# Optimization experiments

Measured on AMD Instinct MI355X. Metric: run time of the kernel, lower is better.

Reference implementation:

```python
import jax, jax.numpy as jnp
import numpy as np

N_NODES = 100000
N_EDGES = 1600000
N_GRAPHS = 128
ATOM_F = 92
BOND_F = 41
EMB = 64
HID = 128
CHG = 16
N_LAYERS = 3
EPS = 1e-5


def setup_inputs() -> dict:
    key = jax.random.key(0)
    ks = jax.random.split(key, 32)
    s = 0.05
    inp = {
        "x": jax.random.normal(ks[0], (N_NODES, ATOM_F), jnp.float32),
        "edge_attr": jax.random.uniform(ks[1], (N_EDGES, BOND_F), jnp.float32),
        "charge": jax.random.normal(ks[2], (N_GRAPHS,), jnp.float32),
        "edge_index": jax.random.randint(ks[3], (2, N_EDGES), 0, N_NODES),
        "batch": jnp.sort(jax.random.randint(ks[4], (N_NODES,), 0, N_GRAPHS)),
        # embeddings
        "W_charge": jax.random.normal(ks[5], (1, CHG), jnp.float32) * s,
        "b_charge": jnp.zeros((CHG,), jnp.float32),
        "W_atom": jax.random.normal(ks[6], (ATOM_F + CHG, EMB), jnp.float32) * s,
        "b_atom": jnp.zeros((EMB,), jnp.float32),
        "W_bond": jax.random.normal(ks[7], (BOND_F, EMB), jnp.float32) * s,
        "b_bond": jnp.zeros((EMB,), jnp.float32),
        # conv layers (stacked over layer dim)
        "conv_eW1": jax.random.normal(ks[8], (N_LAYERS, 3 * EMB, EMB), jnp.float32) * s,
        "conv_eb1": jnp.zeros((N_LAYERS, EMB), jnp.float32),
        "conv_eW2": jax.random.normal(ks[9], (N_LAYERS, EMB, EMB), jnp.float32) * s,
        "conv_eb2": jnp.zeros((N_LAYERS, EMB), jnp.float32),
        "conv_nW1": jax.random.normal(ks[10], (N_LAYERS, 2 * EMB, EMB), jnp.float32) * s,
        "conv_nb1": jnp.zeros((N_LAYERS, EMB), jnp.float32),
        "conv_nW2": jax.random.normal(ks[11], (N_LAYERS, EMB, EMB), jnp.float32) * s,
        "conv_nb2": jnp.zeros((N_LAYERS, EMB), jnp.float32),
        "bn_gamma": jnp.ones((N_LAYERS, EMB), jnp.float32),
        "bn_beta": jnp.zeros((N_LAYERS, EMB), jnp.float32),
        # predictor
        "pW1": jax.random.normal(ks[12], (EMB, HID), jnp.float32) * s,
        "pb1": jnp.zeros((HID,), jnp.float32),
        "pW2": jax.random.normal(ks[13], (HID, HID), jnp.float32) * s,
        "pb2": jnp.zeros((HID,), jnp.float32),
        "pW3": jax.random.normal(ks[14], (HID, 1), jnp.float32) * s,
        "pb3": jnp.zeros((1,), jnp.float32),
    }
    return inp


def reference(x, edge_attr, charge, W_charge, b_charge, W_atom, b_atom,
              W_bond, b_bond, conv_eW1, conv_eb1, conv_eW2, conv_eb2,
              conv_nW1, conv_nb1, conv_nW2, conv_nb2, bn_gamma, bn_beta,
              pW1, pb1, pW2, pb2, pW3, pb3, edge_index, batch):
    sp = jax.nn.softplus
    n_nodes = x.shape[0]
    n_graphs = charge.shape[0]

    # early charge integration: per-graph charge embedding broadcast to nodes
    charge_feat = charge[:, None] @ W_charge + b_charge          # [B, CHG]
    x = jnp.concatenate([x, charge_feat[batch]], axis=1)          # [N, ATOM_F+CHG]
    x = x @ W_atom + b_atom                                       # [N, EMB]
    ea = edge_attr @ W_bond + b_bond                              # [E, EMB]

    row, col = edge_index[0], edge_index[1]
    for i in range(conv_eW1.shape[0]):
        xr, xc = x[row], x[col]                                   # gathers [E, EMB]
        # edge update: MLP on [x_row, x_col, edge_attr]
        e_in = jnp.concatenate([xr, xc, ea], axis=1)              # [E, 3*EMB]
        ea = sp(e_in @ conv_eW1[i] + conv_eb1[i]) @ conv_eW2[i] + conv_eb2[i]
        # node messages: MLP on [x_row, new edge_attr]
        m_in = jnp.concatenate([xr, ea], axis=1)                  # [E, 2*EMB]
        msg = sp(m_in @ conv_nW1[i] + conv_nb1[i]) @ conv_nW2[i] + conv_nb2[i]
        x_new = jax.ops.segment_sum(msg, col, num_segments=n_nodes)
        # BatchNorm1d (training-mode batch stats, biased variance)
        mean = jnp.mean(x_new, axis=0)
        var = jnp.var(x_new, axis=0)
        x_new = (x_new - mean) * jax.lax.rsqrt(var + EPS) * bn_gamma[i] + bn_beta[i]
        x = sp(x_new) + x                                         # residual

    # global mean pool over graphs
    sums = jax.ops.segment_sum(x, batch, num_segments=n_graphs)   # [B, EMB]
    cnt = jax.ops.segment_sum(jnp.ones((n_nodes, 1), x.dtype), batch, num_segments=n_graphs)
    g = sums / jnp.maximum(cnt, 1.0)

    # predictor MLP (dropout is identity in eval mode)
    h = sp(g @ pW1 + pb1)
    h = sp(h @ pW2 + pb2)
    out = h @ pW3 + pb3                                           # [B, 1]
    return out.squeeze(-1)
```

## Files before the change

### kernel.cpp

```cpp
#include <hip/hip_runtime.h>
#include <math.h>

typedef short v8s __attribute__((ext_vector_type(8)));
typedef float v4f __attribute__((ext_vector_type(4)));
typedef unsigned int u32x4 __attribute__((ext_vector_type(4)));

__device__ __forceinline__ u32x4 nt_load4(const void* p) {
  return __builtin_nontemporal_load((const u32x4*)p);
}
__device__ __forceinline__ void nt_store4(void* p, u32x4 v) {
  __builtin_nontemporal_store(v, (u32x4*)p);
}

__device__ __forceinline__ float sp_f(float x) {
  return fmaxf(x, 0.0f) + 0.69314718056f * __log2f(1.0f + __expf(-fabsf(x)));
}

__device__ __forceinline__ unsigned short f2bf(float f) {
  union { float f; unsigned u; } x; x.f = f;
  unsigned r = (x.u + 0x7FFF + ((x.u >> 16) & 1)) >> 16;
  return (unsigned short)r;
}

__device__ __forceinline__ float bf2f(unsigned short h) {
  union { unsigned u; float f; } x; x.u = ((unsigned)h) << 16;
  return x.f;
}

__global__ __launch_bounds__(256) void k_prep_wfrag(
    const float* __restrict__ eW1, const float* __restrict__ eW2,
    const float* __restrict__ nW1, const float* __restrict__ nW2,
    const float* __restrict__ W_bond, unsigned short* __restrict__ wfrag) {
  if (blockIdx.x == 12) {
    unsigned short* out = wfrag + 12 * 4096;
    for (int f = threadIdx.x; f < 4096; f += 256) {
      int j = f & 7, ln = (f >> 3) & 63, kh = (f >> 9) & 1, ct = f >> 10;
      int k = kh * 32 + (ln >> 4) * 8 + j;
      int n = ct * 16 + (ln & 15);
      out[f] = (k < 41) ? f2bf(W_bond[k * 64 + n]) : 0;
    }
    return;
  }
  int i = blockIdx.x >> 2;
  int m = blockIdx.x & 3;
  const float* W;
  if (m == 0)      W = eW1 + (size_t)i * 192 * 64 + 128 * 64;
  else if (m == 1) W = eW2 + (size_t)i * 64 * 64;
  else if (m == 2) W = nW1 + (size_t)i * 128 * 64 + 64 * 64;
  else             W = nW2 + (size_t)i * 64 * 64;
  unsigned short* out = wfrag + ((size_t)i * 4 + m) * 4096;
  for (int f = threadIdx.x; f < 4096; f += 256) {
    int j = f & 7, ln = (f >> 3) & 63, kh = (f >> 9) & 1, ct = f >> 10;
    int k = kh * 32 + (ln >> 4) * 8 + j;
    int n = ct * 16 + (ln & 15);
    out[f] = f2bf(W[k * 64 + n]);
  }
}

__global__ __launch_bounds__(256) void k_embed_nodes(
    const float* __restrict__ x, const int* __restrict__ batch,
    const float* __restrict__ charge, const float* __restrict__ W_charge,
    const float* __restrict__ b_charge, const float* __restrict__ W_atom,
    const float* __restrict__ b_atom, float* __restrict__ xemb, int N) {
  __shared__ float sW[108 * 64];
  __shared__ float sX[128 * 92];
  __shared__ float sb[64];
  __shared__ float sWc[16];
  __shared__ float sbc[16];
  for (int i = threadIdx.x; i < 108 * 64; i += blockDim.x) sW[i] = W_atom[i];
  if (threadIdx.x < 64) sb[threadIdx.x] = b_atom[threadIdx.x];
  if (threadIdx.x < 16) {
    sWc[threadIdx.x] = W_charge[threadIdx.x];
    sbc[threadIdx.x] = b_charge[threadIdx.x];
  }
  int ntiles = (N + 127) >> 7;
  for (int tile = blockIdx.x; tile < ntiles; tile += gridDim.x) {
    int base = tile << 7;
    int cnt = N - base; if (cnt > 128) cnt = 128;
    __syncthreads();
    if (cnt == 128) {
      const u32x4* src = (const u32x4*)(x + (size_t)base * 92);
      for (int i = threadIdx.x; i < 2944; i += 256)
        ((u32x4*)sX)[i] = nt_load4(&src[i]);
    } else {
      for (int i = threadIdx.x; i < cnt * 92; i += 256)
        sX[i] = x[(size_t)base * 92 + i];
    }
    __syncthreads();
    int t = threadIdx.x;
    int node = t & 127, half = t >> 7;
    if (node < cnt) {
      int n = base + node;
      float acc[32];
#pragma unroll
      for (int j = 0; j < 32; ++j) acc[j] = sb[half * 32 + j];
      const float* xr = sX + node * 92;
      for (int k = 0; k < 92; ++k) {
        float a = xr[k];
        const float* wk = sW + k * 64 + half * 32;
#pragma unroll
        for (int j = 0; j < 32; ++j) acc[j] = fmaf(a, wk[j], acc[j]);
      }
      float ch = charge[batch[n]];
#pragma unroll
      for (int c = 0; c < 16; ++c) {
        float cf = fmaf(ch, sWc[c], sbc[c]);
        const float* wk = sW + (92 + c) * 64 + half * 32;
#pragma unroll
        for (int j = 0; j < 32; ++j) acc[j] = fmaf(cf, wk[j], acc[j]);
      }
      float* o = xemb + (size_t)n * 64 + half * 32;
#pragma unroll
      for (int q8 = 0; q8 < 8; ++q8)
        ((float4*)o)[q8] = make_float4(acc[4*q8], acc[4*q8+1], acc[4*q8+2], acc[4*q8+3]);
    }
  }
}

__global__ __launch_bounds__(256) void k_hist(const int* __restrict__ col,
                                              int* __restrict__ counts, int E) {
  int stride = gridDim.x * blockDim.x;
  for (int e = blockIdx.x * blockDim.x + threadIdx.x; e < E; e += stride)
    atomicAdd(&counts[col[e]], 1);
}

__global__ __launch_bounds__(256) void k_scan1(const int* __restrict__ counts,
                                               int* __restrict__ cursor,
                                               int* __restrict__ bsum, int N) {
  __shared__ int sd[2][256];
  int t = threadIdx.x;
  int i = blockIdx.x * 256 + t;
  int v = (i < N) ? counts[i] : 0;
  sd[0][t] = v;
  __syncthreads();
  int s = 0;
#pragma unroll
  for (int off = 1; off < 256; off <<= 1) {
    int nv = sd[s][t];
    if (t >= off) nv += sd[s][t - off];
    sd[s ^ 1][t] = nv;
    s ^= 1;
    __syncthreads();
  }
  if (i < N) cursor[i] = sd[s][t] - v;
  if (t == 255) bsum[blockIdx.x] = sd[s][255];
}

__global__ __launch_bounds__(256) void k_scan2(int* __restrict__ b, int NB) {
  __shared__ int sd[2][256];
  __shared__ int carry_s;
  int t = threadIdx.x;
  if (t == 0) carry_s = 0;
  __syncthreads();
  for (int base = 0; base < NB; base += 256) {
    int i = base + t;
    int v = (i < NB) ? b[i] : 0;
    sd[0][t] = v;
    __syncthreads();
    int s = 0;
#pragma unroll
    for (int off = 1; off < 256; off <<= 1) {
      int nv = sd[s][t];
      if (t >= off) nv += sd[s][t - off];
      sd[s ^ 1][t] = nv;
      s ^= 1;
      __syncthreads();
    }
    int c = carry_s;
    int tot = sd[s][255];
    if (i < NB) b[i] = sd[s][t] + c;
    __syncthreads();
    if (t == 0) carry_s = c + tot;
    __syncthreads();
  }
}

__global__ __launch_bounds__(256) void k_scatter(
    const int* __restrict__ row, const int* __restrict__ col,
    int* __restrict__ cursor, const int* __restrict__ bsum,
    int* __restrict__ pos, int* __restrict__ row_s, int* __restrict__ col_s,
    int E) {
  int stride = gridDim.x * blockDim.x;
  for (int e = blockIdx.x * blockDim.x + threadIdx.x; e < E; e += stride) {
    int c = col[e];
    int p = atomicAdd(&cursor[c], 1);
    p += (c >= 256) ? bsum[(c >> 8) - 1] : 0;
    pos[e] = p;
    row_s[p] = row[e];
    col_s[p] = c;
  }
}

__global__ __launch_bounds__(256) void k_embed_bonds_mfma(
    const float* __restrict__ eattr, const int* __restrict__ pos,
    const unsigned short* __restrict__ gWb, const float* __restrict__ b_bond,
    unsigned short* __restrict__ ea16, int E) {
  __shared__ unsigned short sA[128 * 64];
  __shared__ unsigned short sOut[128 * 64];
  __shared__ float sb[64];
  __shared__ int spos[128];
  int tid = threadIdx.x;
  int w = tid >> 6, l = tid & 63, q = l >> 4, c16 = l & 15;
  int rbase = w * 32;
  if (tid < 64) sb[tid] = b_bond[tid];
  {
    uint4 z = make_uint4(0, 0, 0, 0);
    for (int i = tid; i < 1024; i += 256) ((uint4*)sA)[i] = z;
  }
  int ntiles = (E + 127) >> 7;
  for (int tile = blockIdx.x; tile < ntiles; tile += gridDim.x) {
    int te = tile << 7;
    int cnt = E - te; if (cnt > 128) cnt = 128;
    __syncthreads();
    int nflt = cnt * 41;
    for (int i = tid; i < nflt; i += 256) {
      int r = i / 41, k = i - r * 41;
      float v = __builtin_nontemporal_load(&eattr[(size_t)te * 41 + i]);
      sA[r * 64 + (k ^ ((r & 7) << 3))] = f2bf(v);
    }
    if (tid < 128) spos[tid] = (te + tid < E) ? pos[te + tid] : -1;
    __syncthreads();
    v8s bfr[4][2], af[2][2];
    v4f acc[2][4];
    const v8s* wp_ = (const v8s*)gWb;
#pragma unroll
    for (int ct = 0; ct < 4; ++ct)
#pragma unroll
      for (int kh = 0; kh < 2; ++kh)
        bfr[ct][kh] = wp_[(ct * 2 + kh) * 64 + l];
#pragma unroll
    for (int rb = 0; rb < 2; ++rb)
#pragma unroll
      for (int kh = 0; kh < 2; ++kh) {
        int row_ = rbase + rb * 16 + c16;
        af[rb][kh] = *(const v8s*)&sA[row_ * 64 +
                                      ((kh * 32 + q * 8) ^ ((row_ & 7) << 3))];
      }
#pragma unroll
    for (int rb = 0; rb < 2; ++rb)
#pragma unroll
      for (int ct = 0; ct < 4; ++ct) {
        v4f a_ = {0.f, 0.f, 0.f, 0.f};
        a_ = __builtin_amdgcn_mfma_f32_16x16x32_bf16(af[rb][0], bfr[ct][0], a_, 0, 0, 0);
        a_ = __builtin_amdgcn_mfma_f32_16x16x32_bf16(af[rb][1], bfr[ct][1], a_, 0, 0, 0);
        acc[rb][ct] = a_;
      }
#pragma unroll
    for (int rb = 0; rb < 2; ++rb)
#pragma unroll
      for (int ct = 0; ct < 4; ++ct) {
        int n = ct * 16 + c16;
#pragma unroll
        for (int r = 0; r < 4; ++r) {
          float v = acc[rb][ct][r] + sb[n];
          int row = rbase + rb * 16 + q * 4 + r;
          sOut[row * 64 + (n ^ ((row & 7) << 3))] = f2bf(v);
        }
      }
    __syncthreads();
    for (int i = tid; i < 1024; i += 256) {
      int r = i >> 3, cc = i & 7;
      int p = spos[r];
      if (p >= 0) {
        u32x4 d = *(const u32x4*)&sOut[r * 64 + ((cc * 8) ^ ((r & 7) << 3))];
        nt_store4(&ea16[(size_t)p * 64 + cc * 8], d);
      }
    }
  }
}

__device__ __forceinline__ void node_pre_body(
    const float* __restrict__ xr, const float* sWa, const float* sWb,
    const float* sWp, unsigned short* __restrict__ up16,
    unsigned short* __restrict__ v16, int n) {
  const float4* xr4 = (const float4*)xr;
  float u[64], p[64];
#pragma unroll
  for (int j = 0; j < 64; ++j) { u[j] = 0.f; p[j] = 0.f; }
  for (int k4 = 0; k4 < 16; ++k4) {
    float4 av = xr4[k4];
    const float* wa = sWa + k4 * 256;
    const float* wp = sWp + k4 * 256;
#pragma unroll
    for (int j = 0; j < 64; ++j) u[j] = fmaf(av.x, wa[j], u[j]);
#pragma unroll
    for (int j = 0; j < 64; ++j) p[j] = fmaf(av.x, wp[j], p[j]);
#pragma unroll
    for (int j = 0; j < 64; ++j) u[j] = fmaf(av.y, wa[64 + j], u[j]);
#pragma unroll
    for (int j = 0; j < 64; ++j) p[j] = fmaf(av.y, wp[64 + j], p[j]);
#pragma unroll
    for (int j = 0; j < 64; ++j) u[j] = fmaf(av.z, wa[128 + j], u[j]);
#pragma unroll
    for (int j = 0; j < 64; ++j) p[j] = fmaf(av.z, wp[128 + j], p[j]);
#pragma unroll
    for (int j = 0; j < 64; ++j) u[j] = fmaf(av.w, wa[192 + j], u[j]);
#pragma unroll
    for (int j = 0; j < 64; ++j) p[j] = fmaf(av.w, wp[192 + j], p[j]);
  }
  unsigned short* o = up16 + (size_t)n * 128;
#pragma unroll
  for (int q8 = 0; q8 < 8; ++q8) {
    unsigned short tmp[8];
#pragma unroll
    for (int j = 0; j < 8; ++j) {
      int i = q8 * 8 + j;
      tmp[j] = f2bf(u[((i & 3) << 4) | (i >> 2)]);
    }
    *(uint4*)&o[q8 * 8] = *(uint4*)tmp;
  }
#pragma unroll
  for (int q8 = 0; q8 < 8; ++q8) {
    unsigned short tmp[8];
#pragma unroll
    for (int j = 0; j < 8; ++j) {
      int i = q8 * 8 + j;
      tmp[j] = f2bf(p[((i & 3) << 4) | (i >> 2)]);
    }
    *(uint4*)&o[64 + q8 * 8] = *(uint4*)tmp;
  }
  float vv[64];
#pragma unroll
  for (int j = 0; j < 64; ++j) vv[j] = 0.f;
  for (int k4 = 0; k4 < 16; ++k4) {
    float4 av = xr4[k4];
    const float* wb = sWb + k4 * 256;
#pragma unroll
    for (int j = 0; j < 64; ++j) vv[j] = fmaf(av.x, wb[j], vv[j]);
#pragma unroll
    for (int j = 0; j < 64; ++j) vv[j] = fmaf(av.y, wb[64 + j], vv[j]);
#pragma unroll
    for (int j = 0; j < 64; ++j) vv[j] = fmaf(av.z, wb[128 + j], vv[j]);
#pragma unroll
    for (int j = 0; j < 64; ++j) vv[j] = fmaf(av.w, wb[192 + j], vv[j]);
  }
  unsigned short* ov = v16 + (size_t)n * 64;
#pragma unroll
  for (int q8 = 0; q8 < 8; ++q8) {
    unsigned short tmp[8];
#pragma unroll
    for (int j = 0; j < 8; ++j) {
      int i = q8 * 8 + j;
      tmp[j] = f2bf(vv[((i & 3) << 4) | (i >> 2)]);
    }
    *(uint4*)&ov[q8 * 8] = *(uint4*)tmp;
  }
}

__global__ __launch_bounds__(256) void k_node_pre(
    const float* __restrict__ xemb, const float* __restrict__ eW1,
    const float* __restrict__ nW1, unsigned short* __restrict__ up16,
    unsigned short* __restrict__ v16, float* __restrict__ xnew, int N) {
  __shared__ float sWa[64 * 64];
  __shared__ float sWb[64 * 64];
  __shared__ float sWp[64 * 64];
  for (int i = threadIdx.x; i < 64 * 64; i += blockDim.x) {
    sWa[i] = eW1[i];
    sWb[i] = eW1[64 * 64 + i];
    sWp[i] = nW1[i];
  }
  __syncthreads();
  int stride = gridDim.x * blockDim.x;
  float4 z = make_float4(0.f, 0.f, 0.f, 0.f);
  for (int n = blockIdx.x * blockDim.x + threadIdx.x; n < N; n += stride) {
    node_pre_body(xemb + (size_t)n * 64, sWa, sWb, sWp, up16, v16, n);
    float4* xz = (float4*)(xnew + (size_t)n * 64);
#pragma unroll
    for (int q = 0; q < 16; ++q) xz[q] = z;
  }
}

__global__ __launch_bounds__(256) void k_bn_pre(
    float* __restrict__ xemb, float* __restrict__ xnew,
    const float* __restrict__ bnacc, const float* __restrict__ gamma,
    const float* __restrict__ beta, const float* __restrict__ eW1n,
    const float* __restrict__ nW1n, unsigned short* __restrict__ up16,
    unsigned short* __restrict__ v16, int N) {
  __shared__ float sWa[64 * 64];
  __shared__ float sWb[64 * 64];
  __shared__ float sWp[64 * 64];
  __shared__ float sscale[64], sshift[64];
  for (int i = threadIdx.x; i < 64 * 64; i += blockDim.x) {
    sWa[i] = eW1n[i];
    sWb[i] = eW1n[64 * 64 + i];
    sWp[i] = nW1n[i];
  }
  if (threadIdx.x < 64) {
    float inv = 1.0f / (float)N;
    float m = bnacc[threadIdx.x] * inv;
    float var = bnacc[64 + threadIdx.x] * inv - m * m;
    float rs = rsqrtf(var + 1e-5f);
    float g = gamma[threadIdx.x];
    sscale[threadIdx.x] = rs * g;
    sshift[threadIdx.x] = beta[threadIdx.x] - m * rs * g;
  }
  __syncthreads();
  int stride = gridDim.x * blockDim.x;
  float4 z = make_float4(0.f, 0.f, 0.f, 0.f);
  for (int n = blockIdx.x * blockDim.x + threadIdx.x; n < N; n += stride) {
    float* xr = xemb + (size_t)n * 64;
    float4* xnrow = (float4*)(xnew + (size_t)n * 64);
#pragma unroll
    for (int q = 0; q < 16; ++q) {
      float4 xn4 = xnrow[q];
      float4 xo4 = ((const float4*)xr)[q];
      xo4.x += sp_f(fmaf(xn4.x, sscale[4*q+0], sshift[4*q+0]));
      xo4.y += sp_f(fmaf(xn4.y, sscale[4*q+1], sshift[4*q+1]));
      xo4.z += sp_f(fmaf(xn4.z, sscale[4*q+2], sshift[4*q+2]));
      xo4.w += sp_f(fmaf(xn4.w, sscale[4*q+3], sshift[4*q+3]));
      ((float4*)xr)[q] = xo4;
      xnrow[q] = z;
    }
    node_pre_body(xr, sWa, sWb, sWp, up16, v16, n);
  }
}

#define READ_FRAGS(P)                                                        \
  {                                                                          \
    const v8s* wp_ = (const v8s*)gWf + (P) * 512;                            \
    _Pragma("unroll") for (int ct = 0; ct < 4; ++ct)                         \
        _Pragma("unroll") for (int kh = 0; kh < 2; ++kh)                     \
            bfr[ct][kh] = wp_[(ct * 2 + kh) * 64 + l];                       \
    {                                                                        \
      int row_ = rbase + c16;                                                \
      _Pragma("unroll") for (int kh = 0; kh < 2; ++kh)                       \
        af[kh] = *(const v8s*)&sA[row_ * 64 +                                \
                                  ((kh * 32 + q * 8) ^ ((row_ & 7) << 3))];  \
    }                                                                        \
  }

#define DO_MFMA()                                                            \
  _Pragma("unroll") for (int ct = 0; ct < 4; ++ct) {                         \
    v4f a_ = {0.f, 0.f, 0.f, 0.f};                                           \
    a_ = __builtin_amdgcn_mfma_f32_16x16x32_bf16(af[0], bfr[ct][0], a_,      \
                                                 0, 0, 0);                   \
    a_ = __builtin_amdgcn_mfma_f32_16x16x32_bf16(af[1], bfr[ct][1], a_,      \
                                                 0, 0, 0);                   \
    acc[ct] = a_;                                                            \
  }

__global__ __launch_bounds__(512, 4) void k_edge_mfma(
    const int* __restrict__ row_s, const int* __restrict__ col_s,
    unsigned short* __restrict__ ea16, const unsigned short* __restrict__ up16,
    const unsigned short* __restrict__ v16,
    const unsigned short* __restrict__ gWf, const float* __restrict__ eb1,
    const float* __restrict__ eb2, const float* __restrict__ nb1,
    const float* __restrict__ nb2, float* __restrict__ xnew,
    float* __restrict__ bnacc, int E, int store_ea) {
  __shared__ __align__(16) unsigned char smem[65536];
  unsigned short* sA = (unsigned short*)smem;
  float* msgb        = (float*)smem;
  float* sBb         = (float*)(smem + 32768);
  int* scol          = (int*)(smem + 33792);

  int tid = threadIdx.x;
  int te = blockIdx.x * 128;
  int w = tid >> 6, l = tid & 63, q = l >> 4, c16 = l & 15;
  int rbase = w * 16;

  if (blockIdx.x == 0 && tid < 128) bnacc[tid] = 0.0f;

  int rid[4], cid[4], eid[4];
#pragma unroll
  for (int r = 0; r < 4; ++r) {
    int e = te + rbase + q * 4 + r;
    eid[r] = e;
    int ec = e < E ? e : E - 1;
    rid[r] = row_s[ec];
    cid[r] = col_s[ec];
  }
  ushort4 uu_pf[4], vv_pf[4];
#pragma unroll
  for (int r = 0; r < 4; ++r) {
    uu_pf[r] = *(const ushort4*)&up16[(size_t)rid[r] * 128 + c16 * 4];
    vv_pf[r] = *(const ushort4*)&v16[(size_t)cid[r] * 64 + c16 * 4];
  }

  if (tid < 64) {
    sBb[0 * 64 + tid] = eb1[tid];
    sBb[1 * 64 + tid] = eb2[tid];
    sBb[2 * 64 + tid] = nb1[tid];
    sBb[3 * 64 + tid] = nb2[tid];
  }
  if (tid < 128) {
    int e = te + tid;
    scol[tid] = col_s[e < E ? e : E - 1];
  }
  for (int i = tid; i < 1024; i += 512) {
    int r = i >> 3, cc = i & 7;
    int e = te + r;
    if (e >= E) e = E - 1;
    u32x4 d = nt_load4(&ea16[(size_t)e * 64 + cc * 8]);
    *(u32x4*)&sA[r * 64 + ((cc * 8) ^ ((r & 7) << 3))] = d;
  }

  v8s af[2];
  v8s bfr[4][2];
  v4f acc[4];

  __syncthreads();

  READ_FRAGS(0);
  DO_MFMA();
  ushort4 pp_pf[4];
#pragma unroll
  for (int r = 0; r < 4; ++r)
    pp_pf[r] = *(const ushort4*)&up16[(size_t)rid[r] * 128 + 64 + c16 * 4];
#pragma unroll
  for (int r = 0; r < 4; ++r) {
    const unsigned short* up_ = (const unsigned short*)&uu_pf[r];
    const unsigned short* vp_ = (const unsigned short*)&vv_pf[r];
    int row = rbase + q * 4 + r;
#pragma unroll
    for (int ct = 0; ct < 4; ++ct) {
      int n = ct * 16 + c16;
      float t = acc[ct][r] + sBb[n] + bf2f(up_[ct]) + bf2f(vp_[ct]);
      t = sp_f(t);
      sA[row * 64 + (n ^ ((row & 7) << 3))] = f2bf(t);
    }
  }

  READ_FRAGS(1);
  DO_MFMA();
#pragma unroll
  for (int ct = 0; ct < 4; ++ct) {
    int n = ct * 16 + c16;
#pragma unroll
    for (int r = 0; r < 4; ++r) {
      float en = acc[ct][r] + sBb[64 + n];
      int row = rbase + q * 4 + r;
      sA[row * 64 + (n ^ ((row & 7) << 3))] = f2bf(en);
    }
  }
  if (store_ea) {
    __syncthreads();
    for (int i = tid; i < 1024; i += 512) {
      int r = i >> 3, cc = i & 7;
      if (te + r < E) {
        u32x4 d = *(const u32x4*)&sA[r * 64 + ((cc * 8) ^ ((r & 7) << 3))];
        nt_store4(&ea16[(size_t)(te + r) * 64 + cc * 8], d);
      }
    }
    __syncthreads();
  }

  READ_FRAGS(2);
  DO_MFMA();
#pragma unroll
  for (int r = 0; r < 4; ++r) {
    const unsigned short* pp_ = (const unsigned short*)&pp_pf[r];
    int row = rbase + q * 4 + r;
#pragma unroll
    for (int ct = 0; ct < 4; ++ct) {
      int n = ct * 16 + c16;
      float t2 = acc[ct][r] + sBb[128 + n] + bf2f(pp_[ct]);
      t2 = sp_f(t2);
      sA[row * 64 + (n ^ ((row & 7) << 3))] = f2bf(t2);
    }
  }

  READ_FRAGS(3);
  __syncthreads();
  DO_MFMA();
#pragma unroll
  for (int ct = 0; ct < 4; ++ct) {
    int n = ct * 16 + c16;
#pragma unroll
    for (int r = 0; r < 4; ++r) {
      float msg = acc[ct][r] + sBb[192 + n];
      int row = rbase + q * 4 + r;
      msgb[row * 64 + n] = (eid[r] < E) ? msg : 0.0f;
    }
  }
  __syncthreads();

  int nrows = E - te;
  if (nrows > 128) nrows = 128;
  for (int r0 = w; r0 < nrows; r0 += 8) {
    int c0 = scol[r0];
    if (r0 > 0 && scol[r0 - 1] == c0) continue;
    float s = 0.0f;
    int r = r0;
    do {
      s += msgb[r * 64 + l];
      ++r;
    } while (r < nrows && scol[r] == c0);
    if (r0 > 0 && r < nrows)
      xnew[(size_t)c0 * 64 + l] = s;
    else
      atomicAdd(&xnew[(size_t)c0 * 64 + l], s);
  }
}

__global__ __launch_bounds__(256) void k_bn_stats(
    const float* __restrict__ xnew, float* __restrict__ bnacc, int N) {
  int t = threadIdx.x;
  int ch = t & 63;
  int sl = t >> 6;
  float s = 0.f, s2 = 0.f;
  for (int n = blockIdx.x * 4 + sl; n < N; n += gridDim.x * 4) {
    float v = xnew[(size_t)n * 64 + ch];
    s += v;
    s2 = fmaf(v, v, s2);
  }
  __shared__ float red[256], red2[256];
  red[t] = s;
  red2[t] = s2;
  __syncthreads();
  if (sl == 0) {
    s = red[ch] + red[64 + ch] + red[128 + ch] + red[192 + ch];
    s2 = red2[ch] + red2[64 + ch] + red2[128 + ch] + red2[192 + ch];
    atomicAdd(&bnacc[ch], s);
    atomicAdd(&bnacc[64 + ch], s2);
  }
}

__device__ __forceinline__ int lbound(const int* a, int n, int key) {
  int lo = 0, hi = n;
  while (lo < hi) {
    int mid = (lo + hi) >> 1;
    if (a[mid] < key) lo = mid + 1; else hi = mid;
  }
  return lo;
}

__global__ __launch_bounds__(256) void k_pool_pred_bn(
    const float* __restrict__ x, const float* __restrict__ xnew,
    const float* __restrict__ bnacc, const float* __restrict__ gamma,
    const float* __restrict__ beta, const int* __restrict__ batch, int N,
    const float* __restrict__ pW1, const float* __restrict__ pb1,
    const float* __restrict__ pW2, const float* __restrict__ pb2,
    const float* __restrict__ pW3, const float* __restrict__ pb3,
    float* __restrict__ out) {
  __shared__ float sscale[64], sshift[64];
  int t = threadIdx.x;
  if (t < 64) {
    float inv = 1.0f / (float)N;
    float m = bnacc[t] * inv;
    float var = bnacc[64 + t] * inv - m * m;
    float rs = rsqrtf(var + 1e-5f);
    float g = gamma[t];
    sscale[t] = rs * g;
    sshift[t] = beta[t] - m * rs * g;
  }
  __syncthreads();
  int b = blockIdx.x;
  int lo = lbound(batch, N, b);
  int hi = lbound(batch, N, b + 1);
  int ch = t & 63;
  int sl = t >> 6;
  float sc = sscale[ch], sh = sshift[ch];
  float s = 0.f;
  for (int n = lo + sl; n < hi; n += 4) {
    float xv = x[(size_t)n * 64 + ch];
    float xn = xnew[(size_t)n * 64 + ch];
    s += xv + sp_f(fmaf(xn, sc, sh));
  }
  __shared__ float red4[4][64];
  __shared__ float sg[64];
  __shared__ float sh1[128];
  __shared__ float red[128];
  red4[sl][ch] = s;
  __syncthreads();
  if (t < 64) {
    float tot = red4[0][t] + red4[1][t] + red4[2][t] + red4[3][t];
    float cnt = (float)(hi - lo);
    sg[t] = tot / fmaxf(cnt, 1.0f);
  }
  __syncthreads();
  if (t < 128) {
    float h = pb1[t];
    for (int k = 0; k < 64; ++k) h = fmaf(sg[k], pW1[k * 128 + t], h);
    sh1[t] = sp_f(h);
  }
  __syncthreads();
  if (t < 128) {
    float h = pb2[t];
    for (int k = 0; k < 128; ++k) h = fmaf(sh1[k], pW2[k * 128 + t], h);
    red[t] = sp_f(h) * pW3[t];
  }
  __syncthreads();
  for (int off = 64; off > 0; off >>= 1) {
    if (t < off) red[t] += red[t + off];
    __syncthreads();
  }
  if (t == 0) out[b] = red[0] + pb3[0];
}

extern "C" void kernel_launch(void* const* d_in, const int* in_sizes, int n_in,
                              void* d_out, int out_size, void* d_ws, size_t ws_size,
                              hipStream_t stream) {
  const float* x         = (const float*)d_in[0];
  const float* edge_attr = (const float*)d_in[1];
  const float* charge    = (const float*)d_in[2];
  const int*   eidx      = (const int*)d_in[3];
  const int*   batch     = (const int*)d_in[4];
  const float* W_charge  = (const float*)d_in[5];
  const float* b_charge  = (const float*)d_in[6];
  const float* W_atom    = (const float*)d_in[7];
  const float* b_atom    = (const float*)d_in[8];
  const float* W_bond    = (const float*)d_in[9];
  const float* b_bond    = (const float*)d_in[10];
  const float* eW1 = (const float*)d_in[11];
  const float* eb1 = (const float*)d_in[12];
  const float* eW2 = (const float*)d_in[13];
  const float* eb2 = (const float*)d_in[14];
  const float* nW1 = (const float*)d_in[15];
  const float* nb1 = (const float*)d_in[16];
  const float* nW2 = (const float*)d_in[17];
  const float* nb2 = (const float*)d_in[18];
  const float* gam = (const float*)d_in[19];
  const float* bet = (const float*)d_in[20];
  const float* pW1 = (const float*)d_in[21];
  const float* pb1 = (const float*)d_in[22];
  const float* pW2 = (const float*)d_in[23];
  const float* pb2 = (const float*)d_in[24];
  const float* pW3 = (const float*)d_in[25];
  const float* pb3 = (const float*)d_in[26];

  int N = in_sizes[4];
  int E = in_sizes[3] / 2;
  int B = in_sizes[2];
  const int* row = eidx;
  const int* col = eidx + E;

  char* wptr = (char*)d_ws;
  unsigned short* ea16 = (unsigned short*)wptr; wptr += (((size_t)E * 64 * 2 + 255) & ~255ull);
  unsigned short* up16 = (unsigned short*)wptr; wptr += (((size_t)N * 128 * 2 + 255) & ~255ull);
  unsigned short* v16  = (unsigned short*)wptr; wptr += (((size_t)N * 64 * 2 + 255) & ~255ull);
  unsigned short* wfrag = (unsigned short*)wptr; wptr += 13 * 4096 * 2;
  float* xemb = (float*)wptr; wptr += (size_t)N * 64 * 4;
  float* xnew = (float*)wptr; wptr += (size_t)N * 64 * 4;
  float* bnacc = (float*)wptr; wptr += 256 * 4;
  int* counts = (int*)wptr;   wptr += (size_t)N * 4;
  int* cursor = (int*)wptr;   wptr += (size_t)N * 4;
  int* bsum = (int*)wptr;     wptr += 4096;
  int* pos = (int*)wptr;      wptr += (size_t)E * 4;
  int* row_s = (int*)wptr;    wptr += (size_t)E * 4;
  int* col_s = (int*)wptr;    wptr += (size_t)E * 4;

  int NB = (N + 255) / 256;

  k_prep_wfrag<<<13, 256, 0, stream>>>(eW1, eW2, nW1, nW2, W_bond, wfrag);
  hipMemsetAsync(counts, 0, (size_t)N * 4, stream);
  k_hist<<<2048, 256, 0, stream>>>(col, counts, E);
  k_scan1<<<NB, 256, 0, stream>>>(counts, cursor, bsum, N);
  k_scan2<<<1, 256, 0, stream>>>(bsum, NB);
  k_scatter<<<2048, 256, 0, stream>>>(row, col, cursor, bsum, pos, row_s,
                                      col_s, E);

  int ntilesN = (N + 127) / 128;
  k_embed_nodes<<<ntilesN, 256, 0, stream>>>(x, batch, charge, W_charge,
                                             b_charge, W_atom, b_atom, xemb, N);
  k_embed_bonds_mfma<<<2048, 256, 0, stream>>>(edge_attr, pos,
                                               wfrag + 12 * 4096, b_bond,
                                               ea16, E);
  k_node_pre<<<NB, 256, 0, stream>>>(xemb, eW1, nW1, up16, v16, xnew, N);

  int gridE = (E + 127) / 128;
  for (int i = 0; i < 3; ++i) {
    k_edge_mfma<<<gridE, 512, 0, stream>>>(
        row_s, col_s, ea16, up16, v16, wfrag + (size_t)i * 16384,
        eb1 + (size_t)i * 64, eb2 + (size_t)i * 64, nb1 + (size_t)i * 64,
        nb2 + (size_t)i * 64, xnew, bnacc, E, (i < 2) ? 1 : 0);
    k_bn_stats<<<1024, 256, 0, stream>>>(xnew, bnacc, N);
    if (i < 2) {
      k_bn_pre<<<NB, 256, 0, stream>>>(
          xemb, xnew, bnacc, gam + (size_t)i * 64, bet + (size_t)i * 64,
          eW1 + (size_t)(i + 1) * 192 * 64, nW1 + (size_t)(i + 1) * 128 * 64,
          up16, v16, N);
    }
  }

  k_pool_pred_bn<<<B, 256, 0, stream>>>(xemb, xnew, bnacc, gam + 2 * 64,
                                        bet + 2 * 64, batch, N, pW1, pb1,
                                        pW2, pb2, pW3, pb3, (float*)d_out);
}
```

Measured before the change: 2.040 ms.

## Process two edge tiles per block with double-buffered LDS and cross-tile prefetch

Each edge-kernel block now handles two consecutive 128-edge tiles instead of one, and the grid is halved to match. Both tiles' edge features are loaded into separate LDS buffers up front. The gathered node features for the second tile are prefetched while the first tile's MFMA chain runs. The aim is to hide gather and load latency and amortize per-block setup such as bias loads and bnacc init. The cost is more live registers for the prefetch arrays and half as many blocks to spread across CUs, which may reduce latency hiding from occupancy.

New measurement: 2.175 ms. 1.07x slower.

```diff
diff --git a/kernel.cpp b/kernel.cpp
--- a/kernel.cpp
+++ b/kernel.cpp
@@ -415,7 +415,7 @@
   }
 }
 
-#define READ_FRAGS(P)                                                        \
+#define RFRAGS(P, SAX)                                                       \
   {                                                                          \
     const v8s* wp_ = (const v8s*)gWf + (P) * 512;                            \
     _Pragma("unroll") for (int ct = 0; ct < 4; ++ct)                         \
@@ -424,7 +424,7 @@
     {                                                                        \
       int row_ = rbase + c16;                                                \
       _Pragma("unroll") for (int kh = 0; kh < 2; ++kh)                       \
-        af[kh] = *(const v8s*)&sA[row_ * 64 +                                \
+        af[kh] = *(const v8s*)&(SAX)[row_ * 64 +                             \
                                   ((kh * 32 + q * 8) ^ ((row_ & 7) << 3))];  \
     }                                                                        \
   }
@@ -448,32 +448,39 @@
     const float* __restrict__ nb2, float* __restrict__ xnew,
     float* __restrict__ bnacc, int E, int store_ea) {
   __shared__ __align__(16) unsigned char smem[65536];
-  unsigned short* sA = (unsigned short*)smem;
+  unsigned short* sA0 = (unsigned short*)smem;
   float* msgb        = (float*)smem;
   float* sBb         = (float*)(smem + 32768);
   int* scol          = (int*)(smem + 33792);
+  unsigned short* sA1 = (unsigned short*)(smem + 34816);
 
   int tid = threadIdx.x;
-  int te = blockIdx.x * 128;
   int w = tid >> 6, l = tid & 63, q = l >> 4, c16 = l & 15;
   int rbase = w * 16;
 
   if (blockIdx.x == 0 && tid < 128) bnacc[tid] = 0.0f;
 
-  int rid[4], cid[4], eid[4];
+  int te[2];
+  te[0] = blockIdx.x * 256;
+  te[1] = te[0] + 128;
+
+  int ridA[2][4], cidA[2][4], eidA[2][4];
+#pragma unroll
+  for (int tt = 0; tt < 2; ++tt)
+#pragma unroll
+    for (int r = 0; r < 4; ++r) {
+      int e = te[tt] + rbase + q * 4 + r;
+      eidA[tt][r] = e;
+      int ec = e < E ? e : E - 1;
+      ridA[tt][r] = row_s[ec];
+      cidA[tt][r] = col_s[ec];
+    }
+
+  ushort4 uuA[2][4], vvA[2][4], ppA[2][4];
 #pragma unroll
   for (int r = 0; r < 4; ++r) {
-    int e = te + rbase + q * 4 + r;
-    eid[r] = e;
-    int ec = e < E ? e : E - 1;
-    rid[r] = row_s[ec];
-    cid[r] = col_s[ec];
-  }
-  ushort4 uu_pf[4], vv_pf[4];
-#pragma unroll
-  for (int r = 0; r < 4; ++r) {
-    uu_pf[r] = *(const ushort4*)&up16[(size_t)rid[r] * 128 + c16 * 4];
-    vv_pf[r] = *(const ushort4*)&v16[(size_t)cid[r] * 64 + c16 * 4];
+    uuA[0][r] = *(const ushort4*)&up16[(size_t)ridA[0][r] * 128 + c16 * 4];
+    vvA[0][r] = *(const ushort4*)&v16[(size_t)cidA[0][r] * 64 + c16 * 4];
   }
 
   if (tid < 64) {
@@ -482,16 +489,19 @@
     sBb[2 * 64 + tid] = nb1[tid];
     sBb[3 * 64 + tid] = nb2[tid];
   }
-  if (tid < 128) {
-    int e = te + tid;
+  if (tid < 256) {
+    int tt = tid >> 7;
+    int e = te[tt] + (tid & 127);
     scol[tid] = col_s[e < E ? e : E - 1];
   }
-  for (int i = tid; i < 1024; i += 512) {
-    int r = i >> 3, cc = i & 7;
-    int e = te + r;
+  for (int i = tid; i < 2048; i += 512) {
+    int tt = i >> 10, ii = i & 1023;
+    int r = ii >> 3, cc = ii & 7;
+    int e = te[tt] + r;
     if (e >= E) e = E - 1;
     u32x4 d = nt_load4(&ea16[(size_t)e * 64 + cc * 8]);
-    *(u32x4*)&sA[r * 64 + ((cc * 8) ^ ((r & 7) << 3))] = d;
+    unsigned short* sAx = tt ? sA1 : sA0;
+    *(u32x4*)&sAx[r * 64 + ((cc * 8) ^ ((r & 7) << 3))] = d;
   }
 
   v8s af[2];
@@ -500,95 +510,109 @@
 
   __syncthreads();
 
-  READ_FRAGS(0);
-  DO_MFMA();
-  ushort4 pp_pf[4];
-#pragma unroll
-  for (int r = 0; r < 4; ++r)
-    pp_pf[r] = *(const ushort4*)&up16[(size_t)rid[r] * 128 + 64 + c16 * 4];
-#pragma unroll
-  for (int r = 0; r < 4; ++r) {
-    const unsigned short* up_ = (const unsigned short*)&uu_pf[r];
-    const unsigned short* vp_ = (const unsigned short*)&vv_pf[r];
-    int row = rbase + q * 4 + r;
+#pragma unroll
+  for (int tt = 0; tt < 2; ++tt) {
+    if (tt == 1 && te[1] >= E) break;
+    unsigned short* sAx = tt ? sA1 : sA0;
+    int* scl = scol + tt * 128;
+
+    RFRAGS(0, sAx);
+    DO_MFMA();
+#pragma unroll
+    for (int r = 0; r < 4; ++r)
+      ppA[tt][r] =
+          *(const ushort4*)&up16[(size_t)ridA[tt][r] * 128 + 64 + c16 * 4];
+    if (tt == 0) {
+#pragma unroll
+      for (int r = 0; r < 4; ++r) {
+        uuA[1][r] = *(const ushort4*)&up16[(size_t)ridA[1][r] * 128 + c16 * 4];
+        vvA[1][r] = *(const ushort4*)&v16[(size_t)cidA[1][r] * 64 + c16 * 4];
+      }
+    }
+#pragma unroll
+    for (int r = 0; r < 4; ++r) {
+      const unsigned short* up_ = (const unsigned short*)&uuA[tt][r];
+      const unsigned short* vp_ = (const unsigned short*)&vvA[tt][r];
+      int row = rbase + q * 4 + r;
+#pragma unroll
+      for (int ct = 0; ct < 4; ++ct) {
+        int n = ct * 16 + c16;
+        float t = acc[ct][r] + sBb[n] + bf2f(up_[ct]) + bf2f(vp_[ct]);
+        t = sp_f(t);
+        sAx[row * 64 + (n ^ ((row & 7) << 3))] = f2bf(t);
+      }
+    }
+
+    RFRAGS(1, sAx);
+    DO_MFMA();
 #pragma unroll
     for (int ct = 0; ct < 4; ++ct) {
       int n = ct * 16 + c16;
-      float t = acc[ct][r] + sBb[n] + bf2f(up_[ct]) + bf2f(vp_[ct]);
-      t = sp_f(t);
-      sA[row * 64 + (n ^ ((row & 7) << 3))] = f2bf(t);
-    }
-  }
-
-  READ_FRAGS(1);
-  DO_MFMA();
-#pragma unroll
-  for (int ct = 0; ct < 4; ++ct) {
-    int n = ct * 16 + c16;
+#pragma unroll
+      for (int r = 0; r < 4; ++r) {
+        float en = acc[ct][r] + sBb[64 + n];
+        int row = rbase + q * 4 + r;
+        sAx[row * 64 + (n ^ ((row & 7) << 3))] = f2bf(en);
+      }
+    }
+    if (store_ea) {
+      __syncthreads();
+      for (int i = tid; i < 1024; i += 512) {
+        int r = i >> 3, cc = i & 7;
+        if (te[tt] + r < E) {
+          u32x4 d = *(const u32x4*)&sAx[r * 64 + ((cc * 8) ^ ((r & 7) << 3))];
+          nt_store4(&ea16[(size_t)(te[tt] + r) * 64 + cc * 8], d);
+        }
+      }
+      __syncthreads();
+    }
+
+    RFRAGS(2, sAx);
+    DO_MFMA();
 #pragma unroll
     for (int r = 0; r < 4; ++r) {
-      float en = acc[ct][r] + sBb[64 + n];
+      const unsigned short* pp_ = (const unsigned short*)&ppA[tt][r];
       int row = rbase + q * 4 + r;
-      sA[row * 64 + (n ^ ((row & 7) << 3))] = f2bf(en);
-    }
-  }
-  if (store_ea) {
-    __syncthreads();
-    for (int i = tid; i < 1024; i += 512) {
-      int r = i >> 3, cc = i & 7;
-      if (te + r < E) {
-        u32x4 d = *(const u32x4*)&sA[r * 64 + ((cc * 8) ^ ((r & 7) << 3))];
-        nt_store4(&ea16[(size_t)(te + r) * 64 + cc * 8], d);
-      }
-    }
-    __syncthreads();
-  }
-
-  READ_FRAGS(2);
-  DO_MFMA();
-#pragma unroll
-  for (int r = 0; r < 4; ++r) {
-    const unsigned short* pp_ = (const unsigned short*)&pp_pf[r];
-    int row = rbase + q * 4 + r;
+#pragma unroll
+      for (int ct = 0; ct < 4; ++ct) {
+        int n = ct * 16 + c16;
+        float t2 = acc[ct][r] + sBb[128 + n] + bf2f(pp_[ct]);
+        t2 = sp_f(t2);
+        sAx[row * 64 + (n ^ ((row & 7) << 3))] = f2bf(t2);
+      }
+    }
+
+    RFRAGS(3, sAx);
+    __syncthreads();
+    DO_MFMA();
 #pragma unroll
     for (int ct = 0; ct < 4; ++ct) {
       int n = ct * 16 + c16;
-      float t2 = acc[ct][r] + sBb[128 + n] + bf2f(pp_[ct]);
-      t2 = sp_f(t2);
-      sA[row * 64 + (n ^ ((row & 7) << 3))] = f2bf(t2);
-    }
-  }
-
-  READ_FRAGS(3);
-  __syncthreads();
-  DO_MFMA();
-#pragma unroll
-  for (int ct = 0; ct < 4; ++ct) {
-    int n = ct * 16 + c16;
-#pragma unroll
-    for (int r = 0; r < 4; ++r) {
-      float msg = acc[ct][r] + sBb[192 + n];
-      int row = rbase + q * 4 + r;
-      msgb[row * 64 + n] = (eid[r] < E) ? msg : 0.0f;
-    }
-  }
-  __syncthreads();
-
-  int nrows = E - te;
-  if (nrows > 128) nrows = 128;
-  for (int r0 = w; r0 < nrows; r0 += 8) {
-    int c0 = scol[r0];
-    if (r0 > 0 && scol[r0 - 1] == c0) continue;
-    float s = 0.0f;
-    int r = r0;
-    do {
-      s += msgb[r * 64 + l];
-      ++r;
-    } while (r < nrows && scol[r] == c0);
-    if (r0 > 0 && r < nrows)
-      xnew[(size_t)c0 * 64 + l] = s;
-    else
-      atomicAdd(&xnew[(size_t)c0 * 64 + l], s);
+#pragma unroll
+      for (int r = 0; r < 4; ++r) {
+        float msg = acc[ct][r] + sBb[192 + n];
+        int row = rbase + q * 4 + r;
+        msgb[row * 64 + n] = (eidA[tt][r] < E) ? msg : 0.0f;
+      }
+    }
+    __syncthreads();
+
+    int nrows = E - te[tt];
+    if (nrows > 128) nrows = 128;
+    for (int r0 = w; r0 < nrows; r0 += 8) {
+      int c0 = scl[r0];
+      if (r0 > 0 && scl[r0 - 1] == c0) continue;
+      float s = 0.0f;
+      int r = r0;
+      do {
+        s += msgb[r * 64 + l];
+        ++r;
+      } while (r < nrows && scl[r] == c0);
+      if (r0 > 0 && r < nrows)
+        xnew[(size_t)c0 * 64 + l] = s;
+      else
+        atomicAdd(&xnew[(size_t)c0 * 64 + l], s);
+    }
   }
 }
 
@@ -757,7 +781,8 @@
                                                ea16, E);
   k_node_pre<<<NB, 256, 0, stream>>>(xemb, eW1, nW1, up16, v16, xnew, N);
 
-  int gridE = (E + 127) / 128;
+  int ntilesE = (E + 127) / 128;
+  int gridE = (ntilesE + 1) / 2;
   for (int i = 0; i < 3; ++i) {
     k_edge_mfma<<<gridE, 512, 0, stream>>>(
         row_s, col_s, ea16, up16, v16, wfrag + (size_t)i * 16384,
```
